# Performance work log

Hardware: AMD Instinct MI355X
Metric: run time of the kernel (lower is better)

The kernel has to match this reference:

```python
import jax, jax.numpy as jnp
import numpy as np

N_NODES = 100000
N_EDGES = 1000000
D_FEAT = 64


def setup_inputs() -> dict:
    key = jax.random.key(0)
    k1, k2, k3 = jax.random.split(key, 3)
    embeddings = jax.random.normal(k1, (N_NODES, D_FEAT), dtype=jnp.float32)
    src = jax.random.randint(k2, (N_EDGES,), 0, N_NODES, dtype=jnp.int32)
    dst = jax.random.randint(k3, (N_EDGES,), 0, N_NODES, dtype=jnp.int32)
    return {"embeddings": embeddings, "src": src, "dst": dst}


def reference(embeddings, src, dst):
    # DGL update_all(copy_src('h','m'), mean('m','h')):
    # gather source features per edge, then mean-aggregate by destination.
    msgs = embeddings[src]                                    # [E, D]
    summed = jax.ops.segment_sum(msgs, dst, num_segments=N_NODES)   # [N, D]
    counts = jax.ops.segment_sum(jnp.ones((src.shape[0],), jnp.float32), dst,
                                 num_segments=N_NODES)        # [N]
    # nodes with no in-edges get 0 (DGL mean-of-empty semantics)
    denom = jnp.maximum(counts, 1.0)[:, None]
    return summed / denom
```

## Files before the change

kernel.cpp:

```cpp
#include <hip/hip_runtime.h>
#include <hip/hip_fp16.h>

#define N_NODES 100000
#define N_EDGES 1000000
#define D_FEAT  64

#define BIN_SHIFT 6
#define BIN_NODES 64
#define NBINS ((N_NODES + BIN_NODES - 1) >> BIN_SHIFT)
#define BIN_CAP 1152

#define NCHUNK 128
#define CHUNK_E ((N_EDGES + NCHUNK - 1) / NCHUNK)
#define PCHUNK 7936

#define WS_CNT    0
#define WS_PF     (NBINS * NCHUNK / 2)
#define WS_BUCKET (NBINS * NCHUNK)
#define WS_EMB16  (WS_BUCKET + NCHUNK * PCHUNK)
#define WS_NEEDED ((size_t)(WS_EMB16 + (size_t)N_NODES * D_FEAT / 2) * sizeof(int))

__global__ __launch_bounds__(1024) void prep_kernel(const float* __restrict__ emb,
                                                    const int* __restrict__ src,
                                                    const int* __restrict__ dst,
                                                    int* __restrict__ ws) {
    int tid = threadIdx.x;
    if (blockIdx.x < NCHUNK) {
        __shared__ int h[NBINS];
        __shared__ unsigned short s_bin[CHUNK_E];
        __shared__ int s_pack[CHUNK_E];
        for (int j = tid; j < NBINS; j += 1024) h[j] = 0;
        __syncthreads();
        int c  = blockIdx.x;
        int e0 = c * CHUNK_E;
        int n  = min(N_EDGES, e0 + CHUNK_E) - e0;
        for (int i = tid; i < n; i += 1024) {
            int d = dst[e0 + i], s = src[e0 + i];
            int bin = d >> BIN_SHIFT;
            s_bin[i]  = (unsigned short)bin;
            s_pack[i] = ((d & (BIN_NODES - 1)) << 17) | s;
            atomicAdd(&h[bin], 1);
        }
        __syncthreads();
        unsigned short* CNT = (unsigned short*)(ws + WS_CNT);
        for (int j = tid; j < NBINS; j += 1024)
            CNT[j * NCHUNK + c] = (unsigned short)h[j];
        __syncthreads();
        if (tid < 64) {
            int lane = tid, carry = 0;
            for (int cb = 0; cb < NBINS; cb += 64) {
                int idx = cb + lane;
                int v = (idx < NBINS) ? h[idx] : 0;
                int incl = v;
                #pragma unroll
                for (int o = 1; o < 64; o <<= 1) {
                    int t = __shfl_up(incl, o);
                    if (lane >= o) incl += t;
                }
                if (idx < NBINS) h[idx] = carry + incl - v;
                carry += __shfl(incl, 63);
            }
        }
        __syncthreads();
        unsigned short* PF = (unsigned short*)(ws + WS_PF);
        for (int j = tid; j < NBINS; j += 1024)
            PF[j * NCHUNK + c] = (unsigned short)h[j];
        __syncthreads();
        int* __restrict__ run = ws + WS_BUCKET + c * PCHUNK;
        for (int i = tid; i < n; i += 1024) {
            int slot = atomicAdd(&h[s_bin[i]], 1);
            run[slot] = s_pack[i];
        }
    } else {
        __half2* __restrict__ e16 = (__half2*)(ws + WS_EMB16);
        const float4* __restrict__ e32 = (const float4*)emb;
        const int total4 = N_NODES * D_FEAT / 4;
        int start = (blockIdx.x - NCHUNK) * 1024 + tid;
        for (int i = start; i < total4; i += NCHUNK * 1024) {
            float4 v = e32[i];
            e16[2 * i]     = __floats2half2_rn(v.x, v.y);
            e16[2 * i + 1] = __floats2half2_rn(v.z, v.w);
        }
    }
}

__global__ __launch_bounds__(512) void fused_gather_kernel(const int* __restrict__ ws,
                                                           float* __restrict__ out) {
    __shared__ int s_edges[BIN_CAP];
    __shared__ int s_sorted[BIN_CAP];
    __shared__ int s_rcnt[NCHUNK];
    __shared__ int s_roff[NCHUNK];
    __shared__ int s_rbase[NCHUNK];
    __shared__ int s_hist[BIN_NODES];
    __shared__ int s_off[BIN_NODES];
    __shared__ int s_cur[BIN_NODES];
    __shared__ int s_alloc;

    const char* __restrict__ emb16 = (const char*)(ws + WS_EMB16);
    int b   = blockIdx.x;
    int tid = threadIdx.x;

    if (tid < BIN_NODES) s_hist[tid] = 0;
    if (tid == 0) s_alloc = 0;
    __syncthreads();

    if (tid < NCHUNK) {
        const unsigned short* CNT = (const unsigned short*)(ws + WS_CNT);
        const unsigned short* PF  = (const unsigned short*)(ws + WS_PF);
        int cnt = (int)CNT[b * NCHUNK + tid];
        int pf  = (int)PF[b * NCHUNK + tid];
        s_rcnt[tid]  = cnt;
        s_rbase[tid] = tid * PCHUNK + pf;
        s_roff[tid]  = atomicAdd(&s_alloc, cnt);
    }
    __syncthreads();
    int total = s_alloc;
    if (total > BIN_CAP) total = BIN_CAP;

    {
        int g = tid >> 2, li = tid & 3;
        int cg = s_rcnt[g], og = s_roff[g];
        const int* __restrict__ run = ws + WS_BUCKET + s_rbase[g];
        for (int i = li; i < cg; i += 4) {
            int o = og + i;
            if (o < BIN_CAP) {
                int p = run[i];
                s_edges[o] = p;
                atomicAdd(&s_hist[p >> 17], 1);
            }
        }
    }
    __syncthreads();

    if (tid < 64) {
        int v = s_hist[tid];
        int incl = v;
        #pragma unroll
        for (int o = 1; o < 64; o <<= 1) {
            int t = __shfl_up(incl, o);
            if (tid >= o) incl += t;
        }
        s_off[tid] = incl - v;
        s_cur[tid] = incl - v;
    }
    __syncthreads();

    for (int i = tid; i < total; i += 512) {
        int p = s_edges[i];
        s_sorted[atomicAdd(&s_cur[p >> 17], 1)] = p & 0x1FFFF;
    }
    __syncthreads();

    int wave = tid >> 6, lane = tid & 63;
    int sub  = lane >> 4;
    int fq   = lane & 15;
    const int fb = fq << 3;

    #pragma unroll
    for (int pr = 0; pr < 4; ++pr) {
        int lnA = wave * 8 + pr * 2;
        int lnB = lnA + 1;
        int degA = s_hist[lnA], offA = s_off[lnA];
        int degB = s_hist[lnB], offB = s_off[lnB];

        float4 accA = make_float4(0.f, 0.f, 0.f, 0.f);
        float4 accB = make_float4(0.f, 0.f, 0.f, 0.f);

        int iA = sub, iB = sub;
        for (; iA + 12 < degA; iA += 16) {
            uint2 u0 = *(const uint2*)(emb16 + ((size_t)s_sorted[offA + iA]      << 7) + fb);
            uint2 u1 = *(const uint2*)(emb16 + ((size_t)s_sorted[offA + iA + 4]  << 7) + fb);
            uint2 u2 = *(const uint2*)(emb16 + ((size_t)s_sorted[offA + iA + 8]  << 7) + fb);
            uint2 u3 = *(const uint2*)(emb16 + ((size_t)s_sorted[offA + iA + 12] << 7) + fb);
            float2 f;
            f = __half22float2(*(__half2*)&u0.x); accA.x += f.x; accA.y += f.y;
            f = __half22float2(*(__half2*)&u0.y); accA.z += f.x; accA.w += f.y;
            f = __half22float2(*(__half2*)&u1.x); accA.x += f.x; accA.y += f.y;
            f = __half22float2(*(__half2*)&u1.y); accA.z += f.x; accA.w += f.y;
            f = __half22float2(*(__half2*)&u2.x); accA.x += f.x; accA.y += f.y;
            f = __half22float2(*(__half2*)&u2.y); accA.z += f.x; accA.w += f.y;
            f = __half22float2(*(__half2*)&u3.x); accA.x += f.x; accA.y += f.y;
            f = __half22float2(*(__half2*)&u3.y); accA.z += f.x; accA.w += f.y;
        }
        for (; iB + 12 < degB; iB += 16) {
            uint2 u0 = *(const uint2*)(emb16 + ((size_t)s_sorted[offB + iB]      << 7) + fb);
            uint2 u1 = *(const uint2*)(emb16 + ((size_t)s_sorted[offB + iB + 4]  << 7) + fb);
            uint2 u2 = *(const uint2*)(emb16 + ((size_t)s_sorted[offB + iB + 8]  << 7) + fb);
            uint2 u3 = *(const uint2*)(emb16 + ((size_t)s_sorted[offB + iB + 12] << 7) + fb);
            float2 f;
            f = __half22float2(*(__half2*)&u0.x); accB.x += f.x; accB.y += f.y;
            f = __half22float2(*(__half2*)&u0.y); accB.z += f.x; accB.w += f.y;
            f = __half22float2(*(__half2*)&u1.x); accB.x += f.x; accB.y += f.y;
            f = __half22float2(*(__half2*)&u1.y); accB.z += f.x; accB.w += f.y;
            f = __half22float2(*(__half2*)&u2.x); accB.x += f.x; accB.y += f.y;
            f = __half22float2(*(__half2*)&u2.y); accB.z += f.x; accB.w += f.y;
            f = __half22float2(*(__half2*)&u3.x); accB.x += f.x; accB.y += f.y;
            f = __half22float2(*(__half2*)&u3.y); accB.z += f.x; accB.w += f.y;
        }
        {
            uint2 a0 = make_uint2(0u, 0u), a1 = a0, a2 = a0;
            uint2 b0 = a0, b1 = a0, b2 = a0;
            if (iA < degA)     a0 = *(const uint2*)(emb16 + ((size_t)s_sorted[offA + iA]     << 7) + fb);
            if (iA + 4 < degA) a1 = *(const uint2*)(emb16 + ((size_t)s_sorted[offA + iA + 4] << 7) + fb);
            if (iA + 8 < degA) a2 = *(const uint2*)(emb16 + ((size_t)s_sorted[offA + iA + 8] << 7) + fb);
            if (iB < degB)     b0 = *(const uint2*)(emb16 + ((size_t)s_sorted[offB + iB]     << 7) + fb);
            if (iB + 4 < degB) b1 = *(const uint2*)(emb16 + ((size_t)s_sorted[offB + iB + 4] << 7) + fb);
            if (iB + 8 < degB) b2 = *(const uint2*)(emb16 + ((size_t)s_sorted[offB + iB + 8] << 7) + fb);
            float2 f;
            f = __half22float2(*(__half2*)&a0.x); accA.x += f.x; accA.y += f.y;
            f = __half22float2(*(__half2*)&a0.y); accA.z += f.x; accA.w += f.y;
            f = __half22float2(*(__half2*)&a1.x); accA.x += f.x; accA.y += f.y;
            f = __half22float2(*(__half2*)&a1.y); accA.z += f.x; accA.w += f.y;
            f = __half22float2(*(__half2*)&a2.x); accA.x += f.x; accA.y += f.y;
            f = __half22float2(*(__half2*)&a2.y); accA.z += f.x; accA.w += f.y;
            f = __half22float2(*(__half2*)&b0.x); accB.x += f.x; accB.y += f.y;
            f = __half22float2(*(__half2*)&b0.y); accB.z += f.x; accB.w += f.y;
            f = __half22float2(*(__half2*)&b1.x); accB.x += f.x; accB.y += f.y;
            f = __half22float2(*(__half2*)&b1.y); accB.z += f.x; accB.w += f.y;
            f = __half22float2(*(__half2*)&b2.x); accB.x += f.x; accB.y += f.y;
            f = __half22float2(*(__half2*)&b2.y); accB.z += f.x; accB.w += f.y;
        }

        #pragma unroll
        for (int m = 16; m < 64; m <<= 1) {
            accA.x += __shfl_xor(accA.x, m);  accB.x += __shfl_xor(accB.x, m);
            accA.y += __shfl_xor(accA.y, m);  accB.y += __shfl_xor(accB.y, m);
            accA.z += __shfl_xor(accA.z, m);  accB.z += __shfl_xor(accB.z, m);
            accA.w += __shfl_xor(accA.w, m);  accB.w += __shfl_xor(accB.w, m);
        }

        if (sub == 0) {
            int nodeA = (b << BIN_SHIFT) + lnA;
            int nodeB = (b << BIN_SHIFT) + lnB;
            float invA = 1.0f / (float)max(degA, 1);
            float invB = 1.0f / (float)max(degB, 1);
            accA.x *= invA; accA.y *= invA; accA.z *= invA; accA.w *= invA;
            accB.x *= invB; accB.y *= invB; accB.z *= invB; accB.w *= invB;
            if (nodeA < N_NODES)
                *(float4*)(out + (size_t)nodeA * D_FEAT + fq * 4) = accA;
            if (nodeB < N_NODES)
                *(float4*)(out + (size_t)nodeB * D_FEAT + fq * 4) = accB;
        }
    }
}


__global__ void gcn_zero_kernel(float* __restrict__ out, float* __restrict__ counts) {
    int stride = gridDim.x * blockDim.x;
    int i = blockIdx.x * blockDim.x + threadIdx.x;
    const int total = N_NODES * D_FEAT;
    for (int idx = i; idx < total; idx += stride) out[idx] = 0.0f;
    for (int idx = i; idx < N_NODES; idx += stride) counts[idx] = 0.0f;
}

__global__ void gcn_scatter_kernel(const float* __restrict__ emb,
                                   const int* __restrict__ src,
                                   const int* __restrict__ dst,
                                   float* __restrict__ out,
                                   float* __restrict__ counts) {
    int gid  = blockIdx.x * blockDim.x + threadIdx.x;
    int edge = gid >> 6;
    int lane = gid & 63;
    if (edge >= N_EDGES) return;
    int s = src[edge];
    int d = dst[edge];
    float v = emb[(size_t)s * D_FEAT + lane];
    atomicAdd(&out[(size_t)d * D_FEAT + lane], v);
    if (lane == 0) atomicAdd(&counts[d], 1.0f);
}

__global__ void gcn_norm_kernel(float* __restrict__ out,
                                const float* __restrict__ counts) {
    int i = blockIdx.x * blockDim.x + threadIdx.x;
    if (i >= N_NODES * D_FEAT) return;
    int n = i >> 6;
    float c = counts[n];
    out[i] *= (1.0f / fmaxf(c, 1.0f));
}


extern "C" void kernel_launch(void* const* d_in, const int* in_sizes, int n_in,
                              void* d_out, int out_size, void* d_ws, size_t ws_size,
                              hipStream_t stream) {
    const float* emb = (const float*)d_in[0];
    const int*   src = (const int*)d_in[1];
    const int*   dst = (const int*)d_in[2];
    float* out = (float*)d_out;

    if (ws_size >= WS_NEEDED) {
        int* ws = (int*)d_ws;
        prep_kernel<<<2 * NCHUNK, 1024, 0, stream>>>(emb, src, dst, ws);
        fused_gather_kernel<<<NBINS, 512, 0, stream>>>(ws, out);
    } else {
        float* counts = (float*)d_ws;
        gcn_zero_kernel<<<2048, 256, 0, stream>>>(out, counts);
        const int scatter_blocks = (N_EDGES * 64) / 256;
        gcn_scatter_kernel<<<scatter_blocks, 256, 0, stream>>>(emb, src, dst, out, counts);
        const int norm_blocks = (N_NODES * D_FEAT + 255) / 256;
        gcn_norm_kernel<<<norm_blocks, 256, 0, stream>>>(out, counts);
    }
}
```

Measured before the change: 56.17 us.

## Merge edge binning and fp16 conversion into one block type with more chunks

The prep kernel now splits edges into 256 chunks instead of 128, and every block both bins its chunk of edges and converts its slice of the embeddings to fp16. Before, half the blocks binned and half converted. Binning no longer stages packed edges in shared memory. Instead it reads dst twice from global, once for the histogram and once for the scatter, which cuts LDS use and allows more blocks per CU. The gather kernel adapts its run-loading thread mapping to 2 threads per chunk so it still covers all 256 chunks with 512 threads. The trade-off is extra global reads of dst and more, shorter runs per bin in the gather stage.

```diff
diff --git a/kernel.cpp b/kernel.cpp
--- a/kernel.cpp
+++ b/kernel.cpp
@@ -10,9 +10,10 @@
 #define NBINS ((N_NODES + BIN_NODES - 1) >> BIN_SHIFT)
 #define BIN_CAP 1152
 
-#define NCHUNK 128
+#define NCHUNK 256
 #define CHUNK_E ((N_EDGES + NCHUNK - 1) / NCHUNK)
-#define PCHUNK 7936
+#define PCHUNK 3968
+#define CONV4 (N_NODES * D_FEAT / 4 / NCHUNK)
 
 #define WS_CNT    0
 #define WS_PF     (NBINS * NCHUNK / 2)
@@ -24,59 +25,56 @@
                                                     const int* __restrict__ src,
                                                     const int* __restrict__ dst,
                                                     int* __restrict__ ws) {
+    __shared__ int h[NBINS];
     int tid = threadIdx.x;
-    if (blockIdx.x < NCHUNK) {
-        __shared__ int h[NBINS];
-        __shared__ unsigned short s_bin[CHUNK_E];
-        __shared__ int s_pack[CHUNK_E];
-        for (int j = tid; j < NBINS; j += 1024) h[j] = 0;
-        __syncthreads();
-        int c  = blockIdx.x;
-        int e0 = c * CHUNK_E;
-        int n  = min(N_EDGES, e0 + CHUNK_E) - e0;
-        for (int i = tid; i < n; i += 1024) {
-            int d = dst[e0 + i], s = src[e0 + i];
-            int bin = d >> BIN_SHIFT;
-            s_bin[i]  = (unsigned short)bin;
-            s_pack[i] = ((d & (BIN_NODES - 1)) << 17) | s;
-            atomicAdd(&h[bin], 1);
-        }
-        __syncthreads();
-        unsigned short* CNT = (unsigned short*)(ws + WS_CNT);
-        for (int j = tid; j < NBINS; j += 1024)
-            CNT[j * NCHUNK + c] = (unsigned short)h[j];
-        __syncthreads();
-        if (tid < 64) {
-            int lane = tid, carry = 0;
-            for (int cb = 0; cb < NBINS; cb += 64) {
-                int idx = cb + lane;
-                int v = (idx < NBINS) ? h[idx] : 0;
-                int incl = v;
-                #pragma unroll
-                for (int o = 1; o < 64; o <<= 1) {
-                    int t = __shfl_up(incl, o);
-                    if (lane >= o) incl += t;
-                }
-                if (idx < NBINS) h[idx] = carry + incl - v;
-                carry += __shfl(incl, 63);
+    int c   = blockIdx.x;
+    for (int j = tid; j < NBINS; j += 1024) h[j] = 0;
+    __syncthreads();
+
+    int e0 = c * CHUNK_E, e1 = min(N_EDGES, e0 + CHUNK_E);
+    for (int e = e0 + tid; e < e1; e += 1024)
+        atomicAdd(&h[dst[e] >> BIN_SHIFT], 1);
+    __syncthreads();
+
+    unsigned short* CNT = (unsigned short*)(ws + WS_CNT);
+    for (int j = tid; j < NBINS; j += 1024)
+        CNT[j * NCHUNK + c] = (unsigned short)h[j];
+    __syncthreads();
+
+    if (tid < 64) {
+        int lane = tid, carry = 0;
+        for (int cb = 0; cb < NBINS; cb += 64) {
+            int idx = cb + lane;
+            int v = (idx < NBINS) ? h[idx] : 0;
+            int incl = v;
+            #pragma unroll
+            for (int o = 1; o < 64; o <<= 1) {
+                int t = __shfl_up(incl, o);
+                if (lane >= o) incl += t;
             }
-        }
-        __syncthreads();
-        unsigned short* PF = (unsigned short*)(ws + WS_PF);
-        for (int j = tid; j < NBINS; j += 1024)
-            PF[j * NCHUNK + c] = (unsigned short)h[j];
-        __syncthreads();
-        int* __restrict__ run = ws + WS_BUCKET + c * PCHUNK;
-        for (int i = tid; i < n; i += 1024) {
-            int slot = atomicAdd(&h[s_bin[i]], 1);
-            run[slot] = s_pack[i];
-        }
-    } else {
+            if (idx < NBINS) h[idx] = carry + incl - v;
+            carry += __shfl(incl, 63);
+        }
+    }
+    __syncthreads();
+
+    unsigned short* PF = (unsigned short*)(ws + WS_PF);
+    for (int j = tid; j < NBINS; j += 1024)
+        PF[j * NCHUNK + c] = (unsigned short)h[j];
+    __syncthreads();
+
+    int* __restrict__ run = ws + WS_BUCKET + c * PCHUNK;
+    for (int e = e0 + tid; e < e1; e += 1024) {
+        int d = dst[e], s = src[e];
+        int slot = atomicAdd(&h[d >> BIN_SHIFT], 1);
+        run[slot] = ((d & (BIN_NODES - 1)) << 17) | s;
+    }
+
+    {
         __half2* __restrict__ e16 = (__half2*)(ws + WS_EMB16);
         const float4* __restrict__ e32 = (const float4*)emb;
-        const int total4 = N_NODES * D_FEAT / 4;
-        int start = (blockIdx.x - NCHUNK) * 1024 + tid;
-        for (int i = start; i < total4; i += NCHUNK * 1024) {
+        int st = c * CONV4;
+        for (int i = st + tid; i < st + CONV4; i += 1024) {
             float4 v = e32[i];
             e16[2 * i]     = __floats2half2_rn(v.x, v.y);
             e16[2 * i + 1] = __floats2half2_rn(v.z, v.w);
@@ -118,10 +116,10 @@
     if (total > BIN_CAP) total = BIN_CAP;
 
     {
-        int g = tid >> 2, li = tid & 3;
+        int g = tid >> 1, li = tid & 1;
         int cg = s_rcnt[g], og = s_roff[g];
         const int* __restrict__ run = ws + WS_BUCKET + s_rbase[g];
-        for (int i = li; i < cg; i += 4) {
+        for (int i = li; i < cg; i += 2) {
             int o = og + i;
             if (o < BIN_CAP) {
                 int p = run[i];
@@ -289,7 +287,7 @@
 
     if (ws_size >= WS_NEEDED) {
         int* ws = (int*)d_ws;
-        prep_kernel<<<2 * NCHUNK, 1024, 0, stream>>>(emb, src, dst, ws);
+        prep_kernel<<<NCHUNK, 1024, 0, stream>>>(emb, src, dst, ws);
         fused_gather_kernel<<<NBINS, 512, 0, stream>>>(ws, out);
     } else {
         float* counts = (float*)d_ws;
```

New measurement: 58.27 us. +3.7%, slower.
